# Optimization experiments

Measured on AMD Instinct MI355X. Metric: run time of the kernel, lower is better.

## Reference

```python
import jax, jax.numpy as jnp
import numpy as np

N_STATE = 1024
N_HEAD = 16
B, S = 2, 2048
NEG = -1e9  # finite stand-in for -inf in the additive causal mask


def setup_inputs() -> dict:
    key = jax.random.key(0)
    ks = jax.random.split(key, 8)
    sd = N_STATE ** -0.5
    x = jax.random.normal(ks[0], (B, S, N_STATE), dtype=jnp.float32)
    # additive causal mask, as in Whisper: upper triangle = -inf
    i = jnp.arange(S)
    mask = jnp.where(i[None, :] > i[:, None], NEG, 0.0).astype(jnp.float32)
    return {
        "x": x,
        "mask": mask,
        "Wq": jax.random.normal(ks[1], (N_STATE, N_STATE), jnp.float32) * sd,
        "bq": jax.random.normal(ks[2], (N_STATE,), jnp.float32) * 0.02,
        "Wk": jax.random.normal(ks[3], (N_STATE, N_STATE), jnp.float32) * sd,
        "Wv": jax.random.normal(ks[4], (N_STATE, N_STATE), jnp.float32) * sd,
        "bv": jax.random.normal(ks[5], (N_STATE,), jnp.float32) * 0.02,
        "Wo": jax.random.normal(ks[6], (N_STATE, N_STATE), jnp.float32) * sd,
        "bo": jax.random.normal(ks[7], (N_STATE,), jnp.float32) * 0.02,
    }


def reference(x, mask, Wq, bq, Wk, Wv, bv, Wo, bo):
    B_, S_, D = x.shape
    H = N_HEAD
    hd = D // H
    scale = hd ** -0.25  # applied to both q and k, per the source

    q = (x @ Wq + bq).reshape(B_, S_, H, hd) * scale   # [B,S,H,hd]
    k = (x @ Wk).reshape(B_, S_, H, hd) * scale        # key has no bias
    v = (x @ Wv + bv).reshape(B_, S_, H, hd)

    qk = jnp.einsum("bqhd,bkhd->bhqk", q, k) + mask[:S_, :S_]
    w = jax.nn.softmax(qk.astype(jnp.float32), axis=-1).astype(q.dtype)
    o = jnp.einsum("bhqk,bkhd->bqhd", w, v).reshape(B_, S_, D)
    return o @ Wo + bo
```

## Files before the change

### kernel.cpp

```cpp
#include <hip/hip_runtime.h>
#include <hip/hip_bf16.h>

#define BB 2
#define SS 2048
#define DD 1024
#define HH 16
#define HD 64
#define QKSCALE 0.35355339059327373f
#define QKSCALE_E2 0.42466090144f
#define NEGBIG (-1e9f)

using u16 = unsigned short;
typedef __attribute__((ext_vector_type(8))) short short8;
typedef __attribute__((ext_vector_type(4))) float floatx4;
typedef __attribute__((ext_vector_type(4))) unsigned short ushort4v;

#define GLOBAL_AS __attribute__((address_space(1)))
#define LDS_AS __attribute__((address_space(3)))

__device__ __forceinline__ u16 f2b(float f) {
  union { float f; unsigned u; } v; v.f = f;
  return (u16)((v.u + 0x7fffu + ((v.u >> 16) & 1u)) >> 16);
}

__device__ __forceinline__ u16 bconv(float f) {
  union { __hip_bfloat16 h; u16 u; } cv;
  cv.h = __float2bfloat16(f);
  return cv.u;
}

__device__ __forceinline__ float ex2(float f) {
  return __builtin_amdgcn_exp2f(f);
}

__device__ __forceinline__ floatx4 vmax4(floatx4 a, floatx4 b) {
  return (floatx4){fmaxf(a[0], b[0]), fmaxf(a[1], b[1]),
                   fmaxf(a[2], b[2]), fmaxf(a[3], b[3])};
}

__device__ __forceinline__ void gload_lds16(const void* g, void* l) {
  __builtin_amdgcn_global_load_lds((GLOBAL_AS void*)(g), (LDS_AS void*)(l), 16, 0, 0);
}

__global__ __launch_bounds__(256)
void prep(const float* __restrict__ x, ushort4v* __restrict__ xb,
          const float* __restrict__ s0, const float* __restrict__ s1,
          const float* __restrict__ s2, const float* __restrict__ s3,
          u16* __restrict__ wt) {
  const int id = (int)blockIdx.x;
  const int tid = threadIdx.x;
  if (id < 4096) {
    int i = id * 256 + tid;
    const float4* src = (const float4*)x;
    float4 f = src[i];
    ushort4v o = { f2b(f.x), f2b(f.y), f2b(f.z), f2b(f.w) };
    xb[i] = o;
    return;
  }
  __shared__ float tile[32][33];
  const int local = id - 4096;
  const int z = local >> 10;
  const int rem = local & 1023;
  const int c0 = (rem & 31) * 32;
  const int r0 = (rem >> 5) * 32;
  const float* src = (z == 0) ? s0 : (z == 1) ? s1 : (z == 2) ? s2 : s3;
  u16* d = wt + (size_t)z * 1024 * 1024;
  const int tx = tid & 31, ty = tid >> 5;
#pragma unroll
  for (int i = 0; i < 4; ++i)
    tile[ty + i * 8][tx] = src[(size_t)(r0 + ty + i * 8) * 1024 + c0 + tx];
  __syncthreads();
#pragma unroll
  for (int i = 0; i < 4; ++i)
    d[(size_t)(c0 + ty + i * 8) * 1024 + r0 + tx] = f2b(tile[tx][ty + i * 8]);
}

template <typename OutT>
__global__ __launch_bounds__(256, 3)
void gemm_bt(const u16* __restrict__ A, const u16* __restrict__ Bt,
             OutT* __restrict__ C, const float* __restrict__ bias,
             float scale, int M, int N, int K) {
  const int tid = threadIdx.x;
  const int lane = tid & 63;
  const int w = tid >> 6;
  const int id = (int)blockIdx.x;
  const int swz = (id & 7) * 64 + (id >> 3);
  const int m0 = (swz & 63) * 64;
  const int n0 = (swz >> 6) * 128;
  __shared__ u16 As[2][64 * 64];
  __shared__ u16 Bs[2][128 * 64];
  floatx4 acc[2][4];
#pragma unroll
  for (int i = 0; i < 2; ++i)
#pragma unroll
    for (int j = 0; j < 4; ++j) acc[i][j] = (floatx4){0.f, 0.f, 0.f, 0.f};

  const int wr = (w >> 1) * 32;
  const int wc = (w & 1) * 64;
  const int g = lane >> 4;
  const int lr = lane & 15;
  const size_t strideA = (size_t)K * 2;

  auto stage = [&](int k0, int buf) {
#pragma unroll
    for (int p = 0; p < 2; ++p) {
      int L = tid * 16 + p * 4096;
      int row = L >> 7;
      int cb = (L ^ ((row & 7) << 4)) & 127;
      gload_lds16((const char*)A + (size_t)(m0 + row) * strideA + k0 * 2 + cb,
                  (char*)As[buf] + p * 4096 + w * 1024);
    }
#pragma unroll
    for (int p = 0; p < 4; ++p) {
      int L = tid * 16 + p * 4096;
      int row = L >> 7;
      int cb = (L ^ ((row & 7) << 4)) & 127;
      gload_lds16((const char*)Bt + (size_t)(n0 + row) * strideA + k0 * 2 + cb,
                  (char*)Bs[buf] + p * 4096 + w * 1024);
    }
  };

  const int nsteps = K >> 6;
  stage(0, 0);
  for (int t = 0; t < nsteps; ++t) {
    const int buf = t & 1;
    __syncthreads();
    if (t + 1 < nsteps) stage((t + 1) << 6, buf ^ 1);
    const u16* as = As[buf];
    const u16* bs = Bs[buf];
#pragma unroll
    for (int ks = 0; ks < 2; ++ks) {
      short8 af[2], bf[4];
      const int c0 = ks * 32 + g * 8;
#pragma unroll
      for (int mi = 0; mi < 2; ++mi) {
        int row = wr + mi * 16 + lr;
        af[mi] = *(const short8*)(as + row * 64 + (c0 ^ ((row & 7) << 3)));
      }
#pragma unroll
      for (int ni = 0; ni < 4; ++ni) {
        int row = wc + ni * 16 + lr;
        bf[ni] = *(const short8*)(bs + row * 64 + (c0 ^ ((row & 7) << 3)));
      }
      __builtin_amdgcn_s_setprio(1);
#pragma unroll
      for (int mi = 0; mi < 2; ++mi)
#pragma unroll
        for (int ni = 0; ni < 4; ++ni)
          acc[mi][ni] = __builtin_amdgcn_mfma_f32_16x16x32_bf16(af[mi], bf[ni],
                                                                acc[mi][ni], 0, 0, 0);
      __builtin_amdgcn_s_setprio(0);
    }
  }
#pragma unroll
  for (int ni = 0; ni < 4; ++ni) {
    int col = n0 + wc + ni * 16 + lr;
    float bvv = bias ? bias[col] : 0.f;
#pragma unroll
    for (int mi = 0; mi < 2; ++mi) {
#pragma unroll
      for (int r = 0; r < 4; ++r) {
        int rowg = m0 + wr + mi * 16 + g * 4 + r;
        float val = (acc[mi][ni][r] + bvv) * scale;
        if constexpr (sizeof(OutT) == 4) C[(size_t)rowg * N + col] = val;
        else C[(size_t)rowg * N + col] = (OutT)f2b(val);
      }
    }
  }
}

__global__ __launch_bounds__(256, 4)
void gemm_qkv(const u16* __restrict__ A, const u16* __restrict__ Wt3,
              u16* __restrict__ Out3, u16* __restrict__ Vt,
              const float* __restrict__ bq, const float* __restrict__ bv) {
  const int id = (int)blockIdx.x;
  const int swz = (id & 7) * 96 + (id >> 3);
  const int bx = swz & 31;
  const int rest = swz >> 5;
  const int by = rest & 7;
  const int seg = rest >> 3;
  const u16* Bt = Wt3 + (size_t)seg * 1024 * 1024;
  u16* C = Out3 + (size_t)seg * 4096 * 1024;
  const float* bias = (seg == 0) ? bq : (seg == 2) ? bv : nullptr;
  const float scale = (seg == 2) ? 1.0f : QKSCALE_E2;

  const int tid = threadIdx.x;
  const int lane = tid & 63;
  const int w = tid >> 6;
  const int m0 = bx * 128;
  const int n0 = by * 128;
  __shared__ u16 As[2][64 * 64];
  __shared__ u16 Bs[2][64 * 64];
  floatx4 acc[4][4];
#pragma unroll
  for (int i = 0; i < 4; ++i)
#pragma unroll
    for (int j = 0; j < 4; ++j) acc[i][j] = (floatx4){0.f, 0.f, 0.f, 0.f};
  const int wr = (w >> 1) * 64;
  const int wc = (w & 1) * 64;
  const int g = lane >> 4;
  const int lr = lane & 15;

  auto stage = [&](int k0, int buf) {
#pragma unroll
    for (int p = 0; p < 2; ++p) {
      int L = tid * 16 + p * 4096;
      int lrow = L >> 7;
      int un = (L & 127) ^ ((lrow & 7) << 4);
      int r = lrow * 2 + (un >> 6);
      int cb = un & 63;
      gload_lds16((const char*)A + (size_t)(m0 + r) * 2048 + k0 * 2 + cb,
                  (char*)As[buf] + p * 4096 + w * 1024);
      gload_lds16((const char*)Bt + (size_t)(n0 + r) * 2048 + k0 * 2 + cb,
                  (char*)Bs[buf] + p * 4096 + w * 1024);
    }
  };

  stage(0, 0);
  for (int t = 0; t < 32; ++t) {
    const int buf = t & 1;
    __syncthreads();
    if (t + 1 < 32) stage((t + 1) << 5, buf ^ 1);
    const u16* as = As[buf];
    const u16* bs = Bs[buf];
    short8 af[4], bf[4];
#pragma unroll
    for (int mi = 0; mi < 4; ++mi) {
      int r = wr + mi * 16 + lr;
      af[mi] = *(const short8*)((const char*)as +
               ((r >> 1) * 128 + ((((r & 1) << 6) | (g * 16)) ^ (((r >> 1) & 7) << 4))));
    }
#pragma unroll
    for (int ni = 0; ni < 4; ++ni) {
      int r = wc + ni * 16 + lr;
      bf[ni] = *(const short8*)((const char*)bs +
               ((r >> 1) * 128 + ((((r & 1) << 6) | (g * 16)) ^ (((r >> 1) & 7) << 4))));
    }
    __builtin_amdgcn_s_setprio(1);
#pragma unroll
    for (int mi = 0; mi < 4; ++mi)
#pragma unroll
      for (int ni = 0; ni < 4; ++ni)
        acc[mi][ni] = __builtin_amdgcn_mfma_f32_16x16x32_bf16(af[mi], bf[ni],
                                                              acc[mi][ni], 0, 0, 0);
    __builtin_amdgcn_s_setprio(0);
  }

  if (seg == 2) {
    const int bseg = m0 >> 11;
    const int s0 = (m0 & 2047) + wr + g * 4;
#pragma unroll
    for (int ni = 0; ni < 4; ++ni) {
      int d = n0 + wc + ni * 16 + lr;
      float bvv = bv[d];
      u16* vrow = Vt + (size_t)(bseg * 1024 + d) * 2048;
#pragma unroll
      for (int mi = 0; mi < 4; ++mi) {
        ushort4v pk = { f2b(acc[mi][ni][0] + bvv), f2b(acc[mi][ni][1] + bvv),
                        f2b(acc[mi][ni][2] + bvv), f2b(acc[mi][ni][3] + bvv) };
        *(ushort4v*)(vrow + s0 + mi * 16) = pk;
      }
    }
    return;
  }

  __syncthreads();
  u16* eb = (w == 0) ? (u16*)As[0] : (w == 1) ? (u16*)As[1]
          : (w == 2) ? (u16*)Bs[0] : (u16*)Bs[1];
  const int rr = lane >> 2;
  const int cc = lane & 3;
  float bv4[4];
#pragma unroll
  for (int ni = 0; ni < 4; ++ni)
    bv4[ni] = bias ? bias[n0 + wc + ni * 16 + lr] : 0.f;
#pragma unroll
  for (int mi = 0; mi < 4; ++mi) {
#pragma unroll
    for (int ni = 0; ni < 4; ++ni)
#pragma unroll
      for (int r = 0; r < 4; ++r)
        eb[(g * 4 + r) * 72 + ni * 16 + lr] =
            f2b((acc[mi][ni][r] + bv4[ni]) * scale);
    short8 v0 = *(const short8*)(eb + rr * 72 + cc * 16);
    short8 v1 = *(const short8*)(eb + rr * 72 + cc * 16 + 8);
    u16* dst = C + (size_t)(m0 + wr + mi * 16 + rr) * 1024 + n0 + wc + cc * 16;
    *(short8*)dst = v0;
    *(short8*)(dst + 8) = v1;
  }
}

__device__ __forceinline__ void stream_softmax(floatx4 (&sa)[4], float& m, float& l,
                                               floatx4 (&acc)[4], u16* pl,
                                               bool diag, int wlr, int g, int lr) {
  if (diag) {
#pragma unroll
    for (int ct = 0; ct < 4; ++ct)
#pragma unroll
      for (int r = 0; r < 4; ++r)
        if (ct * 16 + g * 4 + r > wlr) sa[ct][r] += NEGBIG;
  }
  floatx4 v = vmax4(vmax4(sa[0], sa[1]), vmax4(sa[2], sa[3]));
  float mx = fmaxf(fmaxf(v[0], v[1]), fmaxf(v[2], v[3]));
  mx = fmaxf(mx, __shfl_xor(mx, 16, 64));
  mx = fmaxf(mx, __shfl_xor(mx, 32, 64));
  if (!__all(mx <= m + 8.f)) {
    float mn = fmaxf(m, mx);
    float al = ex2(m - mn);
    l *= al;
#pragma unroll
    for (int dt = 0; dt < 4; ++dt) acc[dt] *= al;
    m = mn;
  }
  floatx4 p[4];
#pragma unroll
  for (int ct = 0; ct < 4; ++ct)
#pragma unroll
    for (int r = 0; r < 4; ++r)
      p[ct][r] = ex2(sa[ct][r] - m);
  floatx4 s = (p[0] + p[1]) + (p[2] + p[3]);
  float rs = (s[0] + s[1]) + (s[2] + s[3]);
  rs += __shfl_xor(rs, 16, 64);
  rs += __shfl_xor(rs, 32, 64);
  l += rs;
#pragma unroll
  for (int ct = 0; ct < 4; ++ct) {
    ushort4v pk = { bconv(p[ct][0]), bconv(p[ct][1]),
                    bconv(p[ct][2]), bconv(p[ct][3]) };
    *(ushort4v*)((char*)pl + ((lr * 128 + ct * 32 + g * 8) ^ ((lr & 7) << 4))) = pk;
  }
}

__global__ __launch_bounds__(256, 4)
void flash_attn(const u16* __restrict__ q, const u16* __restrict__ k,
                const u16* __restrict__ vt, u16* __restrict__ o) {
  const int tid = threadIdx.x;
  const int lane = tid & 63;
  const int w = tid >> 6;
  const int g = lane >> 4;
  const int lr = lane & 15;
  const int i = (int)blockIdx.x;
  const int x = i & 7;
  const int kk = i >> 3;
  const int s = kk & 3;
  const int mI = kk >> 2;
  const int u = mI >> 3;
  const int v = mI & 7;
  const int gg = x * 4 + s;
  const int b = gg >> 4;
  const int h = gg & 15;
  const int a = (u + s) & 3;
  const int qt = (a == 0) ? v : (a == 1) ? (31 - v) : (a == 2) ? (16 + v) : (15 - v);
  const int row0 = qt * 64 + w * 16;
  const int wlr = w * 16 + lr;

  __shared__ u16 Ks[2][64 * 64];
  __shared__ u16 Vs[2][64 * 64];
  __shared__ u16 Pl[4][16 * 64];

  short8 qf[2];
  {
    const u16* qp = q + (size_t)(b * SS + row0 + lr) * DD + h * HD + g * 8;
    qf[0] = *(const short8*)qp;
    qf[1] = *(const short8*)(qp + 32);
  }
  floatx4 acc[4];
#pragma unroll
  for (int dt = 0; dt < 4; ++dt) acc[dt] = (floatx4){0.f, 0.f, 0.f, 0.f};
  float m = -1e30f, l = 0.f;

  const char* kbase = (const char*)(k + (size_t)(b * SS) * DD + h * HD);
  const char* vbase = (const char*)(vt + (size_t)((b * HH + h) * HD) * SS);
  const int nt = qt + 1;

  auto stage = [&](int t, int buf) {
    const int kvb = t * 64;
#pragma unroll
    for (int p = 0; p < 2; ++p) {
      int L = tid * 16 + p * 4096;
      int row = L >> 7;
      int cb = (L ^ ((row & 7) << 4)) & 127;
      gload_lds16(kbase + (size_t)(kvb + row) * (DD * 2) + cb,
                  (char*)Ks + buf * 8192 + p * 4096 + w * 1024);
      gload_lds16(vbase + (size_t)row * (SS * 2) + kvb * 2 + cb,
                  (char*)Vs + buf * 8192 + p * 4096 + w * 1024);
    }
  };

  stage(0, 0);
  int cur = 0;
  for (int t = 0; t < nt; ++t) {
    __syncthreads();
    if (t + 1 < nt) stage(t + 1, cur ^ 1);
    const u16* kc = Ks[cur];
    const u16* vc = Vs[cur];

    floatx4 sa[4];
#pragma unroll
    for (int ct = 0; ct < 4; ++ct) sa[ct] = (floatx4){0.f, 0.f, 0.f, 0.f};
    __builtin_amdgcn_s_setprio(1);
#pragma unroll
    for (int ks = 0; ks < 2; ++ks) {
      const int c0 = ks * 32 + g * 8;
#pragma unroll
      for (int ct = 0; ct < 4; ++ct) {
        int row = ct * 16 + lr;
        short8 kf = *(const short8*)(kc + row * 64 + (c0 ^ ((row & 7) << 3)));
        sa[ct] = __builtin_amdgcn_mfma_f32_16x16x32_bf16(kf, qf[ks], sa[ct], 0, 0, 0);
      }
    }
    __builtin_amdgcn_s_setprio(0);

    stream_softmax(sa, m, l, acc, Pl[w], t == qt, wlr, g, lr);

    __builtin_amdgcn_s_setprio(1);
#pragma unroll
    for (int ks = 0; ks < 2; ++ks) {
      const int c0 = ks * 32 + g * 8;
      int pby = (lr * 128 + ks * 64 + g * 16) ^ ((lr & 7) << 4);
      short8 pf = *(const short8*)((const char*)Pl[w] + pby);
#pragma unroll
      for (int dt = 0; dt < 4; ++dt) {
        int row = dt * 16 + lr;
        short8 vf = *(const short8*)(vc + row * 64 + (c0 ^ ((row & 7) << 3)));
        acc[dt] = __builtin_amdgcn_mfma_f32_16x16x32_bf16(vf, pf, acc[dt], 0, 0, 0);
      }
    }
    __builtin_amdgcn_s_setprio(0);
    cur ^= 1;
  }

  float inv = 1.0f / l;
#pragma unroll
  for (int dt = 0; dt < 4; ++dt) {
    ushort4v pa = { bconv(acc[dt][0] * inv), bconv(acc[dt][1] * inv),
                    bconv(acc[dt][2] * inv), bconv(acc[dt][3] * inv) };
    *(ushort4v*)(o + (size_t)(b * SS + row0 + lr) * DD + h * HD + dt * 16 + g * 4) = pa;
  }
}

extern "C" void kernel_launch(void* const* d_in, const int* in_sizes, int n_in,
                              void* d_out, int out_size, void* d_ws, size_t ws_size,
                              hipStream_t stream) {
  const float* x  = (const float*)d_in[0];
  const float* Wq = (const float*)d_in[2];
  const float* bq = (const float*)d_in[3];
  const float* Wk = (const float*)d_in[4];
  const float* Wv = (const float*)d_in[5];
  const float* bv = (const float*)d_in[6];
  const float* Wo = (const float*)d_in[7];
  const float* bo = (const float*)d_in[8];
  float* out = (float*)d_out;

  char* ws = (char*)d_ws;
  u16* xb  = (u16*)(ws);
  u16* wt  = (u16*)(ws + (8u << 20));
  u16* qkv = (u16*)(ws + (16u << 20));
  u16* vtb = (u16*)(ws + (40u << 20));
  u16* ob  = (u16*)(ws + (48u << 20));
  u16* wot = wt + 3u * 1024 * 1024;

  prep<<<8192, 256, 0, stream>>>(x, (ushort4v*)xb, Wq, Wk, Wv, Wo, wt);
  gemm_qkv<<<768, 256, 0, stream>>>(xb, wt, qkv, vtb, bq, bv);
  flash_attn<<<1024, 256, 0, stream>>>(qkv, qkv + (size_t)4096 * 1024, vtb, ob);
  gemm_bt<float><<<512, 256, 0, stream>>>(ob, wot, out, bo, 1.0f,
                                          4096, 1024, 1024);
}
```

Baseline: 107.0 us.

## Split long causal query tiles across two KV halves and merge with a combine kernel

Query tiles in the upper half of each causal sequence (16..31) are now handled by two blocks, each covering half of the KV range. Each half writes unnormalized fp32 partial outputs plus its running max and sum to workspace, and a new combine kernel merges them with a log-sum-exp rescale before writing bf16. The goal is to cap per-block work so the long-tail blocks no longer dominate the attention kernel. In exchange it adds an extra launch, fp32 partial traffic, and reuses workspace regions (xb, Wq area, V section of qkv) that are assumed dead by this point.

```diff
diff --git a/kernel.cpp b/kernel.cpp
--- a/kernel.cpp
+++ b/kernel.cpp
@@ -332,24 +332,34 @@
 
 __global__ __launch_bounds__(256, 4)
 void flash_attn(const u16* __restrict__ q, const u16* __restrict__ k,
-                const u16* __restrict__ vt, u16* __restrict__ o) {
+                const u16* __restrict__ vt, u16* __restrict__ o,
+                float* __restrict__ O0, float* __restrict__ O1,
+                float* __restrict__ mlb) {
   const int tid = threadIdx.x;
   const int lane = tid & 63;
   const int w = tid >> 6;
   const int g = lane >> 4;
   const int lr = lane & 15;
-  const int i = (int)blockIdx.x;
-  const int x = i & 7;
-  const int kk = i >> 3;
-  const int s = kk & 3;
-  const int mI = kk >> 2;
-  const int u = mI >> 3;
-  const int v = mI & 7;
-  const int gg = x * 4 + s;
-  const int b = gg >> 4;
-  const int h = gg & 15;
-  const int a = (u + s) & 3;
-  const int qt = (a == 0) ? v : (a == 1) ? (31 - v) : (a == 2) ? (16 + v) : (15 - v);
+  const int id = (int)blockIdx.x;
+  const int x = id & 7;
+  const int j = id >> 3;
+  const int head = x * 4 + (j / 48);
+  const int e = j % 48;
+  int qt, t0, t1, half;
+  bool split;
+  if (e < 16) {
+    qt = e; t0 = 0; t1 = qt + 1; split = false; half = 0;
+  } else {
+    int e2 = e - 16;
+    qt = 16 + (e2 >> 1);
+    half = e2 & 1;
+    split = true;
+    int mid = (qt + 1) >> 1;
+    t0 = half ? mid : 0;
+    t1 = half ? (qt + 1) : mid;
+  }
+  const int b = head >> 4;
+  const int h = head & 15;
   const int row0 = qt * 64 + w * 16;
   const int wlr = w * 16 + lr;
 
@@ -370,7 +380,6 @@
 
   const char* kbase = (const char*)(k + (size_t)(b * SS) * DD + h * HD);
   const char* vbase = (const char*)(vt + (size_t)((b * HH + h) * HD) * SS);
-  const int nt = qt + 1;
 
   auto stage = [&](int t, int buf) {
     const int kvb = t * 64;
@@ -386,11 +395,11 @@
     }
   };
 
-  stage(0, 0);
+  stage(t0, 0);
   int cur = 0;
-  for (int t = 0; t < nt; ++t) {
+  for (int t = t0; t < t1; ++t) {
     __syncthreads();
-    if (t + 1 < nt) stage(t + 1, cur ^ 1);
+    if (t + 1 < t1) stage(t + 1, cur ^ 1);
     const u16* kc = Ks[cur];
     const u16* vc = Vs[cur];
 
@@ -429,12 +438,48 @@
     cur ^= 1;
   }
 
-  float inv = 1.0f / l;
-#pragma unroll
-  for (int dt = 0; dt < 4; ++dt) {
-    ushort4v pa = { bconv(acc[dt][0] * inv), bconv(acc[dt][1] * inv),
-                    bconv(acc[dt][2] * inv), bconv(acc[dt][3] * inv) };
-    *(ushort4v*)(o + (size_t)(b * SS + row0 + lr) * DD + h * HD + dt * 16 + g * 4) = pa;
+  if (!split) {
+    float inv = 1.0f / l;
+#pragma unroll
+    for (int dt = 0; dt < 4; ++dt) {
+      ushort4v pa = { bconv(acc[dt][0] * inv), bconv(acc[dt][1] * inv),
+                      bconv(acc[dt][2] * inv), bconv(acc[dt][3] * inv) };
+      *(ushort4v*)(o + (size_t)(b * SS + row0 + lr) * DD + h * HD + dt * 16 + g * 4) = pa;
+    }
+  } else {
+    const int prow = (head << 10) + (row0 - 1024) + lr;
+    float* Op = half ? O1 : O0;
+#pragma unroll
+    for (int dt = 0; dt < 4; ++dt)
+      *(floatx4*)(Op + (size_t)prow * 64 + dt * 16 + g * 4) = acc[dt];
+    if (g == 0) {
+      mlb[prow * 4 + half * 2 + 0] = m;
+      mlb[prow * 4 + half * 2 + 1] = l;
+    }
+  }
+}
+
+__global__ __launch_bounds__(256)
+void combine(const float* __restrict__ O0, const float* __restrict__ O1,
+             const float* __restrict__ mlb, u16* __restrict__ o) {
+  const int tid = threadIdx.x;
+  const int d = tid & 63;
+  const int rsub = tid >> 6;
+  const int rbase = (int)blockIdx.x * 64;
+#pragma unroll 4
+  for (int it = 0; it < 16; ++it) {
+    int row = rbase + it * 4 + rsub;
+    float m1 = mlb[row * 4 + 0], l1 = mlb[row * 4 + 1];
+    float m2 = mlb[row * 4 + 2], l2 = mlb[row * 4 + 3];
+    float M = fmaxf(m1, m2);
+    float a1 = ex2(m1 - M), a2 = ex2(m2 - M);
+    float v1 = O0[(size_t)row * 64 + d];
+    float v2 = O1[(size_t)row * 64 + d];
+    float val = (a1 * v1 + a2 * v2) / (a1 * l1 + a2 * l2);
+    int head = row >> 10;
+    int s = 1024 + (row & 1023);
+    int bb = head >> 4, hh = head & 15;
+    o[(size_t)(bb * SS + s) * DD + hh * HD + d] = bconv(val);
   }
 }
 
@@ -458,10 +503,15 @@
   u16* vtb = (u16*)(ws + (40u << 20));
   u16* ob  = (u16*)(ws + (48u << 20));
   u16* wot = wt + 3u * 1024 * 1024;
+  float* O0  = (float*)ws;
+  float* O1  = (float*)(ws + (32u << 20));
+  float* mlb = (float*)(ws + (8u << 20));
 
   prep<<<8192, 256, 0, stream>>>(x, (ushort4v*)xb, Wq, Wk, Wv, Wo, wt);
   gemm_qkv<<<768, 256, 0, stream>>>(xb, wt, qkv, vtb, bq, bv);
-  flash_attn<<<1024, 256, 0, stream>>>(qkv, qkv + (size_t)4096 * 1024, vtb, ob);
+  flash_attn<<<1536, 256, 0, stream>>>(qkv, qkv + (size_t)4096 * 1024, vtb, ob,
+                                       O0, O1, mlb);
+  combine<<<512, 256, 0, stream>>>(O0, O1, mlb, ob);
   gemm_bt<float><<<512, 256, 0, stream>>>(ob, wot, out, bo, 1.0f,
                                           4096, 1024, 1024);
 }
```

Result: slower. 116.1 us (+8.5%).
